# Optimization experiments

Measured on AMD Instinct MI355X. Metric: run time of the kernel, lower is better.

## Reference

```python
import jax, jax.numpy as jnp
import numpy as np

N_NODES = 100000
N_EDGES = 1000000
N_GRAPHS = 2048
MOL_DIM = 9
HID = 64


def setup_inputs() -> dict:
    key = jax.random.key(0)
    ks = jax.random.split(key, 16)
    x = jax.random.normal(ks[0], (N_NODES, MOL_DIM), dtype=jnp.float32)
    edge_src = jax.random.randint(ks[1], (N_EDGES,), 0, N_NODES)
    edge_dst = jax.random.randint(ks[2], (N_EDGES,), 0, N_NODES)
    batch = jnp.sort(jax.random.randint(ks[3], (N_NODES,), 0, N_GRAPHS))
    def lin(k, fan_in, fan_out):
        bound = 1.0 / np.sqrt(fan_in)
        kw, kb = jax.random.split(k)
        W = jax.random.uniform(kw, (fan_in, fan_out), minval=-bound, maxval=bound, dtype=jnp.float32)
        b = jax.random.uniform(kb, (fan_out,), minval=-bound, maxval=bound, dtype=jnp.float32)
        return W, b
    W1, b1 = lin(ks[4], MOL_DIM, HID)
    W2, b2 = lin(ks[5], HID, HID)
    W3, b3 = lin(ks[6], HID, HID)
    Wp1, bp1 = lin(ks[7], 2 * HID, 64)
    Wp2, bp2 = lin(ks[8], 64, 1)
    return dict(x=x, edge_src=edge_src, edge_dst=edge_dst, batch=batch,
                W1=W1, b1=b1, W2=W2, b2=b2, W3=W3, b3=b3,
                Wp1=Wp1, bp1=bp1, Wp2=Wp2, bp2=bp2)


def gcn_conv(x, edge_src, edge_dst, W, b):
    # PyG GCNConv: add self-loops, symmetric D^-1/2 (A+I) D^-1/2 normalization.
    n = x.shape[0]
    h = x @ W  # [N, out]
    ones = jnp.ones_like(edge_dst, dtype=h.dtype)
    deg = jax.ops.segment_sum(ones, edge_dst, num_segments=n) + 1.0  # self-loop counted
    dinv = jax.lax.rsqrt(deg)
    norm = dinv[edge_src] * dinv[edge_dst]  # [E]
    msg = h[edge_src] * norm[:, None]       # gather + scale
    agg = jax.ops.segment_sum(msg, edge_dst, num_segments=n)
    agg = agg + h * (1.0 / deg)[:, None]    # self-loop contribution (norm = 1/deg)
    return agg + b


def reference(x, edge_src, edge_dst, batch, W1, b1, W2, b2, W3, b3, Wp1, bp1, Wp2, bp2):
    h = jax.nn.relu(gcn_conv(x, edge_src, edge_dst, W1, b1))
    h = jax.nn.relu(gcn_conv(h, edge_src, edge_dst, W2, b2))
    h = jax.nn.relu(gcn_conv(h, edge_src, edge_dst, W3, b3))
    # global mean / max pool by graph id
    counts = jax.ops.segment_sum(jnp.ones((h.shape[0],), h.dtype), batch, num_segments=N_GRAPHS)
    sums = jax.ops.segment_sum(h, batch, num_segments=N_GRAPHS)
    mean = sums / jnp.maximum(counts, 1.0)[:, None]
    mx = jax.ops.segment_max(h, batch, num_segments=N_GRAPHS)
    mx = jnp.where(counts[:, None] > 0, mx, 0.0)
    g = jnp.concatenate([mean, mx], axis=1)  # [G, 128]
    # predictor (dropout inactive in eval mode)
    out = jax.nn.relu(g @ Wp1 + bp1) @ Wp2 + bp2
    return out
```

## Files before the change

### kernel.cpp

```cpp
#include <hip/hip_runtime.h>

#define NN 100000
#define NE 1000000
#define NG 2048
#define NBLK 98
#define CSRCAP 2600000

__device__ __forceinline__ float rl(float v, int k) {
    return __int_as_float(__builtin_amdgcn_readlane(__float_as_int(v), k));
}
__device__ __forceinline__ int rli(int v, int k) {
    return __builtin_amdgcn_readlane(v, k);
}

#define PDEG(c) (max(16, ((c) + 7) & ~7))


__global__ void k_cnt(const int* __restrict__ dst, int* __restrict__ cnt,
                      int* __restrict__ ticket,
                      const int* __restrict__ batch, int* __restrict__ pcnt) {
    int i = blockIdx.x * blockDim.x + threadIdx.x;
    if (i < NE) ticket[i] = atomicAdd(&cnt[dst[i]], 1);
    if (i < NN) atomicAdd(&pcnt[batch[i]], 1);
}

__global__ void k_scan1(const int* __restrict__ cnt, int* __restrict__ bsum,
                        const float* __restrict__ x, float* __restrict__ dinv,
                        float* __restrict__ px, float* __restrict__ p1,
                        float* __restrict__ p2) {
    int t = threadIdx.x;
    int base = blockIdx.x * 1024 + t * 4;
    int4 v = {0, 0, 0, 0};
    if (base < NN) v = *(const int4*)(cnt + base);
    int s = PDEG(v.x) + PDEG(v.y) + PDEG(v.z) + PDEG(v.w);
    #pragma unroll
    for (int off = 32; off; off >>= 1) s += __shfl_down(s, off, 64);
    __shared__ int ws[4];
    if ((t & 63) == 0) ws[t >> 6] = s;
    __syncthreads();
    if (t == 0) bsum[blockIdx.x] = ws[0] + ws[1] + ws[2] + ws[3];

    if (base < NN) {
        int c[4] = {v.x, v.y, v.z, v.w};
        #pragma unroll
        for (int j2 = 0; j2 < 4; ++j2) {
            int nd = base + j2;
            float dv = rsqrtf((float)(c[j2] + 1));
            dinv[nd] = dv;
            #pragma unroll
            for (int j = 0; j < 9; ++j) px[nd * 16 + j] = x[nd * 9 + j] * dv;
        }
    } else if (base == NN) {
        #pragma unroll
        for (int j = 0; j < 9; ++j) px[NN * 16 + j] = 0.f;
        for (int j = 0; j < 64; ++j) {
            p1[(size_t)NN * 64 + j] = 0.f;
            p2[(size_t)NN * 64 + j] = 0.f;
        }
    }
}

__global__ void k_scan2(const int* __restrict__ bsum, int* __restrict__ boff, int nb) {
    __shared__ int buf[128];
    int t = threadIdx.x;
    int v = (t < nb) ? bsum[t] : 0;
    buf[t] = v;
    __syncthreads();
    for (int off = 1; off < 128; off <<= 1) {
        int u = (t >= off) ? buf[t - off] : 0;
        __syncthreads();
        buf[t] += u;
        __syncthreads();
    }
    if (t < nb) boff[t] = buf[t] - v;
}

__global__ void k_scan3(const int* __restrict__ cnt, const int* __restrict__ boff,
                        int* __restrict__ prp, int n) {
    int t = threadIdx.x;
    int base = blockIdx.x * 1024 + t * 4;
    int4 v = {0, 0, 0, 0};
    if (base < n) v = *(const int4*)(cnt + base);
    int p0 = PDEG(v.x), p1 = PDEG(v.y), p2 = PDEG(v.z), p3 = PDEG(v.w);
    int s = p0 + p1 + p2 + p3;
    int lane = t & 63;
    int ps = s;
    #pragma unroll
    for (int off = 1; off < 64; off <<= 1) {
        int u = __shfl_up(ps, off, 64);
        if (lane >= off) ps += u;
    }
    __shared__ int ws[4];
    if (lane == 63) ws[t >> 6] = ps;
    __syncthreads();
    int w = t >> 6;
    int woff = 0;
    for (int i = 0; i < 4; ++i) woff += (i < w) ? ws[i] : 0;
    int excl = boff[blockIdx.x] + woff + ps - s;
    if (base < n) {
        prp[base] = excl;          excl += p0;
        prp[base + 1] = excl;      excl += p1;
        prp[base + 2] = excl;      excl += p2;
        prp[base + 3] = excl;      excl += p3;
        if (base + 4 == n) prp[n] = excl;
    }
}

__global__ void k_padinit(int* __restrict__ csr) {
    int i = blockIdx.x * blockDim.x + threadIdx.x;
    if (i * 4 < CSRCAP) {
        int4 v = {NN, NN, NN, NN};
        *(int4*)(csr + i * 4) = v;
    }
}

__global__ void k_fill(const int* __restrict__ src, const int* __restrict__ dst,
                       const int* __restrict__ prp, const int* __restrict__ ticket,
                       int* __restrict__ csr, int E) {
    int i = blockIdx.x * blockDim.x + threadIdx.x;
    if (i < E) csr[prp[dst[i]] + ticket[i]] = src[i];
}


template <int KD, int STRIDE, int POOL>
__global__ __launch_bounds__(256, 6)
void k_layer(const float* __restrict__ pin, const float* __restrict__ W,
             const float* __restrict__ bias, const float* __restrict__ dinv,
             const int* __restrict__ csr, const int* __restrict__ prp,
             const int* __restrict__ batch,
             float* __restrict__ pout, float* __restrict__ psum,
             float* __restrict__ pmax) {
    __shared__ float Ws[KD * 64];
    int tid = threadIdx.x;
    for (int i = tid; i < KD * 64; i += 256) Ws[i] = W[i];
    __syncthreads();
    int f = tid & 63;
    int wv = tid >> 6;
    int n0 = (blockIdx.x * 4 + wv) * 8;
    int fi = (KD < 64) ? ((f < KD) ? f : (KD - 1)) : f;

    int myrp = prp[n0 + min(f, 8)];

#define CHUNK(A0, A1, E0) { \
    int s0 = csr[(E0) + 0], s1 = csr[(E0) + 1], s2 = csr[(E0) + 2], s3 = csr[(E0) + 3]; \
    int s4 = csr[(E0) + 4], s5 = csr[(E0) + 5], s6 = csr[(E0) + 6], s7 = csr[(E0) + 7]; \
    float v0 = pin[(size_t)s0 * STRIDE + fi], v1 = pin[(size_t)s1 * STRIDE + fi]; \
    float v2 = pin[(size_t)s2 * STRIDE + fi], v3 = pin[(size_t)s3 * STRIDE + fi]; \
    float v4 = pin[(size_t)s4 * STRIDE + fi], v5 = pin[(size_t)s5 * STRIDE + fi]; \
    float v6 = pin[(size_t)s6 * STRIDE + fi], v7 = pin[(size_t)s7 * STRIDE + fi]; \
    A0 += (v0 + v2) + (v4 + v6); \
    A1 += (v1 + v3) + (v5 + v7); \
}

    float q0, q1, q2, q3, q4, q5, q6, q7;
#define PAIR(JA, JB, QA, QB) { \
    int ndA = n0 + (JA), ndB = n0 + (JB); \
    int pbA = rli(myrp, JA), peA = rli(myrp, (JA) + 1); \
    int pbB = rli(myrp, JB), peB = rli(myrp, (JB) + 1); \
    float aA0 = pin[(size_t)ndA * STRIDE + fi], aA1 = 0.f; \
    float aB0 = pin[(size_t)ndB * STRIDE + fi], aB1 = 0.f; \
    CHUNK(aA0, aA1, pbA) \
    CHUNK(aB0, aB1, pbB) \
    CHUNK(aA0, aA1, pbA + 8) \
    CHUNK(aB0, aB1, pbB + 8) \
    for (int e = pbA + 16; e < peA; e += 8) CHUNK(aA0, aA1, e) \
    for (int e = pbB + 16; e < peB; e += 8) CHUNK(aB0, aB1, e) \
    QA = (aA0 + aA1) * dinv[ndA]; \
    QB = (aB0 + aB1) * dinv[ndB]; \
}
    PAIR(0, 1, q0, q1)
    PAIR(2, 3, q2, q3)
    PAIR(4, 5, q4, q5)
    PAIR(6, 7, q6, q7)
#undef PAIR
#undef CHUNK

    float bv = bias[f];
    float o0 = bv, o1 = bv, o2 = bv, o3 = bv, o4 = bv, o5 = bv, o6 = bv, o7 = bv;
    #pragma unroll
    for (int k = 0; k < KD; ++k) {
        float wsv = Ws[k * 64 + f];
        o0 = fmaf(rl(q0, k), wsv, o0);
        o1 = fmaf(rl(q1, k), wsv, o1);
        o2 = fmaf(rl(q2, k), wsv, o2);
        o3 = fmaf(rl(q3, k), wsv, o3);
        o4 = fmaf(rl(q4, k), wsv, o4);
        o5 = fmaf(rl(q5, k), wsv, o5);
        o6 = fmaf(rl(q6, k), wsv, o6);
        o7 = fmaf(rl(q7, k), wsv, o7);
    }

    if (POOL == 0) {
#define STORE(O, J) pout[(size_t)(n0 + (J)) * 64 + f] = fmaxf(O, 0.f) * dinv[n0 + (J)];
        STORE(o0, 0) STORE(o1, 1) STORE(o2, 2) STORE(o3, 3)
        STORE(o4, 4) STORE(o5, 5) STORE(o6, 6) STORE(o7, 7)
#undef STORE
    } else {
        int g = batch[n0];
        float sum = 0.f, mx = 0.f;
#define ACCP(O, J) { \
    float r = fmaxf(O, 0.f); \
    int gj = batch[n0 + (J)]; \
    if (gj != g) { \
        atomicAdd(&psum[g * 64 + f], sum); \
        atomicMax((int*)&pmax[g * 64 + f], __float_as_int(mx)); \
        g = gj; sum = 0.f; mx = 0.f; \
    } \
    sum += r; mx = fmaxf(mx, r); \
}
        ACCP(o0, 0) ACCP(o1, 1) ACCP(o2, 2) ACCP(o3, 3)
        ACCP(o4, 4) ACCP(o5, 5) ACCP(o6, 6) ACCP(o7, 7)
#undef ACCP
        atomicAdd(&psum[g * 64 + f], sum);
        atomicMax((int*)&pmax[g * 64 + f], __float_as_int(mx));
    }
}


__global__ void k_pred(const float* __restrict__ psum, const float* __restrict__ pmax,
                       const int* __restrict__ pcnt,
                       const float* __restrict__ Wp1, const float* __restrict__ bp1,
                       const float* __restrict__ Wp2, const float* __restrict__ bp2,
                       float* __restrict__ out, int G) {
    __shared__ float gs[4][128];
    int tid = threadIdx.x;
    int li = tid >> 6;
    int lane = tid & 63;
    int gi = blockIdx.x * 4 + li;
    if (gi < G) {
        float c = fmaxf((float)pcnt[gi], 1.0f);
        gs[li][lane] = psum[gi * 64 + lane] / c;
        gs[li][64 + lane] = pmax[gi * 64 + lane];
    }
    __syncthreads();
    if (gi >= G) return;
    float acc = bp1[lane];
    #pragma unroll
    for (int k = 0; k < 128; ++k) acc += gs[li][k] * Wp1[k * 64 + lane];
    acc = fmaxf(acc, 0.f);
    float r = acc * Wp2[lane];
    #pragma unroll
    for (int off = 32; off; off >>= 1) r += __shfl_down(r, off, 64);
    if (lane == 0) out[gi] = r + bp2[0];
}


extern "C" void kernel_launch(void* const* d_in, const int* in_sizes, int n_in,
                              void* d_out, int out_size, void* d_ws, size_t ws_size,
                              hipStream_t stream) {
    const float* x    = (const float*)d_in[0];
    const int*   esrc = (const int*)d_in[1];
    const int*   edst = (const int*)d_in[2];
    const int*   batch= (const int*)d_in[3];
    const float* W1 = (const float*)d_in[4];  const float* b1 = (const float*)d_in[5];
    const float* W2 = (const float*)d_in[6];  const float* b2 = (const float*)d_in[7];
    const float* W3 = (const float*)d_in[8];  const float* b3 = (const float*)d_in[9];
    const float* Wp1= (const float*)d_in[10]; const float* bp1= (const float*)d_in[11];
    const float* Wp2= (const float*)d_in[12]; const float* bp2= (const float*)d_in[13];
    float* out = (float*)d_out;

    char* ws = (char*)d_ws;
    int*   cnt     = (int*)  (ws + 0);
    float* psum    = (float*)(ws + 400000);
    float* pmax    = (float*)(ws + 924288);
    int*   pcnt    = (int*)  (ws + 1448576);
    const size_t ZBYTES = 1456768;
    float* dinv    = (float*)(ws + 1456768);
    int*   prp     = (int*)  (ws + 1856768);
    int*   bsum    = (int*)  (ws + 2257408);
    int*   boff    = (int*)  (ws + 2257920);
    int*   csr_pad = (int*)  (ws + 2258432);
    float* p1      = (float*)(ws + 12658432);
    float* p2      = (float*)(ws + 38258688);
    int*   ticket  = (int*)  (ws + 12658432);
    float* px      = (float*)(ws + 38258688);

    hipMemsetAsync(ws, 0, ZBYTES, stream);

    k_cnt    <<<(NE + 255) / 256, 256, 0, stream>>>(edst, cnt, ticket, batch, pcnt);
    k_scan1  <<<NBLK, 256, 0, stream>>>(cnt, bsum, x, dinv, px, p1, p2);
    k_scan2  <<<1, 128, 0, stream>>>(bsum, boff, NBLK);
    k_scan3  <<<NBLK, 256, 0, stream>>>(cnt, boff, prp, NN);
    k_padinit<<<(CSRCAP / 4 + 255) / 256, 256, 0, stream>>>(csr_pad);
    k_fill   <<<(NE + 255) / 256, 256, 0, stream>>>(esrc, edst, prp, ticket, csr_pad, NE);

    int nbl = NN / 32;
    k_layer<9, 16, 0><<<nbl, 256, 0, stream>>>(px, W1, b1, dinv, csr_pad, prp, batch, p1, psum, pmax);
    k_layer<64, 64, 0><<<nbl, 256, 0, stream>>>(p1, W2, b2, dinv, csr_pad, prp, batch, p2, psum, pmax);
    k_layer<64, 64, 1><<<nbl, 256, 0, stream>>>(p2, W3, b3, dinv, csr_pad, prp, batch, p1, psum, pmax);

    k_pred <<<(NG + 3) / 4, 256, 0, stream>>>(psum, pmax, pcnt, Wp1, bp1, Wp2, bp2, out, NG);
}
```

Baseline: 247.0 us.

## Fuse block-offset scan and CSR padding init into the prefix-scan kernel

Merges the single-block scan of block sums into each scan3 block, so every block redundantly scans the 98 block totals in shared memory. It also writes only the padding slots of each padded CSR row (sentinel NN) instead of initializing the whole CSR buffer in a separate kernel. This removes two kernel launches and a full-buffer write pass. The layer kernel's launch bounds are raised to 7 blocks per CU, which may tighten the register budget.

Result: slower. 258.7 us (+4.7%).

```diff
diff --git a/kernel.cpp b/kernel.cpp
--- a/kernel.cpp
+++ b/kernel.cpp
@@ -60,28 +60,26 @@
     }
 }
 
-__global__ void k_scan2(const int* __restrict__ bsum, int* __restrict__ boff, int nb) {
+__global__ void k_scan3(const int* __restrict__ cnt, const int* __restrict__ bsum,
+                        int* __restrict__ prp, int* __restrict__ csr, int n) {
     __shared__ int buf[128];
     int t = threadIdx.x;
-    int v = (t < nb) ? bsum[t] : 0;
-    buf[t] = v;
+    if (t < 128) buf[t] = (t < NBLK) ? bsum[t] : 0;
     __syncthreads();
     for (int off = 1; off < 128; off <<= 1) {
-        int u = (t >= off) ? buf[t - off] : 0;
+        int u = 0;
+        if (t < 128 && t >= off) u = buf[t - off];
         __syncthreads();
-        buf[t] += u;
+        if (t < 128) buf[t] += u;
         __syncthreads();
     }
-    if (t < nb) boff[t] = buf[t] - v;
-}
-
-__global__ void k_scan3(const int* __restrict__ cnt, const int* __restrict__ boff,
-                        int* __restrict__ prp, int n) {
-    int t = threadIdx.x;
+    int boff = buf[blockIdx.x] - bsum[blockIdx.x];
+
     int base = blockIdx.x * 1024 + t * 4;
     int4 v = {0, 0, 0, 0};
     if (base < n) v = *(const int4*)(cnt + base);
-    int p0 = PDEG(v.x), p1 = PDEG(v.y), p2 = PDEG(v.z), p3 = PDEG(v.w);
+    int c0 = v.x, c1 = v.y, c2 = v.z, c3 = v.w;
+    int p0 = PDEG(c0), p1 = PDEG(c1), p2 = PDEG(c2), p3 = PDEG(c3);
     int s = p0 + p1 + p2 + p3;
     int lane = t & 63;
     int ps = s;
@@ -90,27 +88,21 @@
         int u = __shfl_up(ps, off, 64);
         if (lane >= off) ps += u;
     }
-    __shared__ int ws[4];
-    if (lane == 63) ws[t >> 6] = ps;
+    __shared__ int wsum[4];
+    if (lane == 63) wsum[t >> 6] = ps;
     __syncthreads();
     int w = t >> 6;
     int woff = 0;
-    for (int i = 0; i < 4; ++i) woff += (i < w) ? ws[i] : 0;
-    int excl = boff[blockIdx.x] + woff + ps - s;
+    for (int i = 0; i < 4; ++i) woff += (i < w) ? wsum[i] : 0;
+    int excl = boff + woff + ps - s;
     if (base < n) {
-        prp[base] = excl;          excl += p0;
-        prp[base + 1] = excl;      excl += p1;
-        prp[base + 2] = excl;      excl += p2;
-        prp[base + 3] = excl;      excl += p3;
-        if (base + 4 == n) prp[n] = excl;
-    }
-}
-
-__global__ void k_padinit(int* __restrict__ csr) {
-    int i = blockIdx.x * blockDim.x + threadIdx.x;
-    if (i * 4 < CSRCAP) {
-        int4 v = {NN, NN, NN, NN};
-        *(int4*)(csr + i * 4) = v;
+        int e0 = excl, e1 = e0 + p0, e2 = e1 + p1, e3 = e2 + p2;
+        prp[base] = e0; prp[base + 1] = e1; prp[base + 2] = e2; prp[base + 3] = e3;
+        if (base + 4 == n) prp[n] = e3 + p3;
+        for (int e = e0 + c0; e < e0 + p0; ++e) csr[e] = NN;
+        for (int e = e1 + c1; e < e1 + p1; ++e) csr[e] = NN;
+        for (int e = e2 + c2; e < e2 + p2; ++e) csr[e] = NN;
+        for (int e = e3 + c3; e < e3 + p3; ++e) csr[e] = NN;
     }
 }
 
@@ -123,7 +115,7 @@
 
 
 template <int KD, int STRIDE, int POOL>
-__global__ __launch_bounds__(256, 6)
+__global__ __launch_bounds__(256, 7)
 void k_layer(const float* __restrict__ pin, const float* __restrict__ W,
              const float* __restrict__ bias, const float* __restrict__ dinv,
              const int* __restrict__ csr, const int* __restrict__ prp,
@@ -268,7 +260,6 @@
     float* dinv    = (float*)(ws + 1456768);
     int*   prp     = (int*)  (ws + 1856768);
     int*   bsum    = (int*)  (ws + 2257408);
-    int*   boff    = (int*)  (ws + 2257920);
     int*   csr_pad = (int*)  (ws + 2258432);
     float* p1      = (float*)(ws + 12658432);
     float* p2      = (float*)(ws + 38258688);
@@ -277,12 +268,10 @@
 
     hipMemsetAsync(ws, 0, ZBYTES, stream);
 
-    k_cnt    <<<(NE + 255) / 256, 256, 0, stream>>>(edst, cnt, ticket, batch, pcnt);
-    k_scan1  <<<NBLK, 256, 0, stream>>>(cnt, bsum, x, dinv, px, p1, p2);
-    k_scan2  <<<1, 128, 0, stream>>>(bsum, boff, NBLK);
-    k_scan3  <<<NBLK, 256, 0, stream>>>(cnt, boff, prp, NN);
-    k_padinit<<<(CSRCAP / 4 + 255) / 256, 256, 0, stream>>>(csr_pad);
-    k_fill   <<<(NE + 255) / 256, 256, 0, stream>>>(esrc, edst, prp, ticket, csr_pad, NE);
+    k_cnt  <<<(NE + 255) / 256, 256, 0, stream>>>(edst, cnt, ticket, batch, pcnt);
+    k_scan1<<<NBLK, 256, 0, stream>>>(cnt, bsum, x, dinv, px, p1, p2);
+    k_scan3<<<NBLK, 256, 0, stream>>>(cnt, bsum, prp, csr_pad, NN);
+    k_fill <<<(NE + 255) / 256, 256, 0, stream>>>(esrc, edst, prp, ticket, csr_pad, NE);
 
     int nbl = NN / 32;
     k_layer<9, 16, 0><<<nbl, 256, 0, stream>>>(px, W1, b1, dinv, csr_pad, prp, batch, p1, psum, pmax);
```
